# Performance work log

Hardware: AMD Instinct MI355X
Metric: run time of the kernel (lower is better)

## Reference

```python
import jax, jax.numpy as jnp
import numpy as np

B, T, F = 512, 1024, 8
H1, H2 = 70, 21   # '80k' config, bidirectional
D1, D2 = 30, 20


def _u(key, shape, fan):
    s = 1.0 / np.sqrt(fan)
    return jax.random.uniform(key, shape, jnp.float32, -s, s)


def setup_inputs() -> dict:
    key = jax.random.key(0)
    ks = iter(jax.random.split(key, 32))
    inp = {"x": jax.random.normal(next(ks), (B, T, F), jnp.float32)}
    # LSTM layer 1 (input F -> H1), forward and backward directions; torch gate order i,f,g,o
    for d in ("f", "b"):
        inp[f"w_ih1_{d}"] = _u(next(ks), (4 * H1, F), H1)
        inp[f"w_hh1_{d}"] = _u(next(ks), (4 * H1, H1), H1)
        inp[f"b_ih1_{d}"] = _u(next(ks), (4 * H1,), H1)
        inp[f"b_hh1_{d}"] = _u(next(ks), (4 * H1,), H1)
    # LSTM layer 2 (input 2*H1 -> H2)
    for d in ("f", "b"):
        inp[f"w_ih2_{d}"] = _u(next(ks), (4 * H2, 2 * H1), H2)
        inp[f"w_hh2_{d}"] = _u(next(ks), (4 * H2, H2), H2)
        inp[f"b_ih2_{d}"] = _u(next(ks), (4 * H2,), H2)
        inp[f"b_hh2_{d}"] = _u(next(ks), (4 * H2,), H2)
    # Dense head: 2*H2 -> D1 -> D2 -> 1
    inp["d1_w"] = _u(next(ks), (D1, 2 * H2), 2 * H2)
    inp["d1_b"] = _u(next(ks), (D1,), 2 * H2)
    inp["d2_w"] = _u(next(ks), (D2, D1), D1)
    inp["d2_b"] = _u(next(ks), (D2,), D1)
    inp["out_w"] = _u(next(ks), (1, D2), D2)
    inp["out_b"] = _u(next(ks), (1,), D2)
    return inp


def _lstm_dir(x, w_ih, w_hh, b_ih, b_hh, reverse):
    # x: [B, T, Fin]; torch LSTM gate order: i, f, g, o
    if reverse:
        x = x[:, ::-1]
    H = w_hh.shape[1]
    pre = jnp.einsum('btf,gf->btg', x, w_ih) + b_ih + b_hh  # [B, T, 4H]
    pre_t = jnp.moveaxis(pre, 1, 0)                          # [T, B, 4H]

    def step(carry, p):
        h, c = carry
        g = p + h @ w_hh.T
        i, f, gg, o = jnp.split(g, 4, axis=-1)
        c = jax.nn.sigmoid(f) * c + jax.nn.sigmoid(i) * jnp.tanh(gg)
        h = jax.nn.sigmoid(o) * jnp.tanh(c)
        return (h, c), h

    init = (jnp.zeros((x.shape[0], H), x.dtype), jnp.zeros((x.shape[0], H), x.dtype))
    _, hs = jax.lax.scan(step, init, pre_t)
    hs = jnp.moveaxis(hs, 0, 1)  # [B, T, H]
    if reverse:
        hs = hs[:, ::-1]
    return hs


def _bilstm(x, wf, uf, bif, bhf, wb, ub, bib, bhb):
    return jnp.concatenate([
        _lstm_dir(x, wf, uf, bif, bhf, reverse=False),
        _lstm_dir(x, wb, ub, bib, bhb, reverse=True),
    ], axis=-1)


def reference(x,
              w_ih1_f, w_hh1_f, b_ih1_f, b_hh1_f,
              w_ih1_b, w_hh1_b, b_ih1_b, b_hh1_b,
              w_ih2_f, w_hh2_f, b_ih2_f, b_hh2_f,
              w_ih2_b, w_hh2_b, b_ih2_b, b_hh2_b,
              d1_w, d1_b, d2_w, d2_b, out_w, out_b):
    h = _bilstm(x, w_ih1_f, w_hh1_f, b_ih1_f, b_hh1_f,
                w_ih1_b, w_hh1_b, b_ih1_b, b_hh1_b)   # [B, T, 2*H1]
    h = _bilstm(h, w_ih2_f, w_hh2_f, b_ih2_f, b_hh2_f,
                w_ih2_b, w_hh2_b, b_ih2_b, b_hh2_b)   # [B, T, 2*H2]
    h = jax.nn.relu(h @ d1_w.T + d1_b)
    h = jax.nn.relu(h @ d2_w.T + d2_b)
    return h @ out_w.T + out_b                          # [B, T, 1]
```

## Files before the change

### kernel.cpp

```cpp
#include <hip/hip_runtime.h>


typedef _Float16 v2f16 __attribute__((ext_vector_type(2)));
typedef _Float16 v4h   __attribute__((ext_vector_type(4)));
typedef _Float16 v8h   __attribute__((ext_vector_type(8)));
typedef float    f32x4 __attribute__((ext_vector_type(4)));

__device__ __forceinline__ float fdot2(v2f16 a, v2f16 b, float c) {
  return __builtin_amdgcn_fdot2(a, b, c, false);
}
#if __has_builtin(__builtin_amdgcn_rcpf)
__device__ __forceinline__ float rcpf(float x) { return __builtin_amdgcn_rcpf(x); }
#else
__device__ __forceinline__ float rcpf(float x) { return 1.f / x; }
#endif
__device__ __forceinline__ float ex2(float v) {
#if __has_builtin(__builtin_amdgcn_exp2f)
  return __builtin_amdgcn_exp2f(v);
#else
  return __expf(v * 0.6931471805599453f);
#endif
}
__device__ __forceinline__ float dpp_xor1(float v) {
  return __builtin_bit_cast(float,
      __builtin_amdgcn_update_dpp(0, __builtin_bit_cast(int, v),
                                  0xB1 , 0xF, 0xF, true));
}

__device__ __forceinline__ void lds_barrier() {
  asm volatile("s_waitcnt lgkmcnt(0)" ::: "memory");
  __builtin_amdgcn_s_barrier();
  __builtin_amdgcn_sched_barrier(0);
}

#define LOG2E  1.4426950408889634f
#define LOG2E2 2.8853900817779268f

#define O_W1M  0u
#define O_WP2  110592u
#define O_W2M  118656u
#define O_BIAS 177792u
#define O_DATA 178496u

__global__ void pack_kernel(const float* __restrict__ wihf, const float* __restrict__ whhf,
                            const float* __restrict__ wihb, const float* __restrict__ whhb,
                            const float* __restrict__ b1if, const float* __restrict__ b1hf,
                            const float* __restrict__ b1ib, const float* __restrict__ b1hb,
                            const float* __restrict__ wih2f, const float* __restrict__ wih2b,
                            const float* __restrict__ whh2f, const float* __restrict__ whh2b,
                            const float* __restrict__ bif, const float* __restrict__ bhf,
                            const float* __restrict__ bib, const float* __restrict__ bhb,
                            char* __restrict__ ws) {
  _Float16* w1m = (_Float16*)(ws + O_W1M);
  _Float16* wp2 = (_Float16*)(ws + O_WP2);
  _Float16* w2m = (_Float16*)(ws + O_W2M);
  float* biasc = (float*)(ws + O_BIAS);
  int idx = blockIdx.x * 256 + threadIdx.x;
  if (idx < 55296) {
    int d = idx / 27648, rem = idx % 27648, rp = rem / 96, k = rem % 96;
    int u = rp >> 2, g = rp & 3;
    const float* wih = d ? wihb : wihf;
    const float* whh = d ? whhb : whhf;
    const float* bi = d ? b1ib : b1if;
    const float* bh = d ? b1hb : b1hf;
    float v = 0.f;
    if (u < 70) {
      int src = g * 70 + u;
      float scale = (g == 2) ? LOG2E2 : LOG2E;
      if (k < 8) v = wih[src * 8 + k] * scale;
      else if (k < 78) v = whh[src * 70 + (k - 8)] * scale;
      else if (k == 78) v = (bi[src] + bh[src]) * scale;
    }
    w1m[idx] = (_Float16)v;
  } else if (idx < 59328) {
    int j = idx - 55296;
    int d = j / 2016, rem = j % 2016, r = rem / 24, k = rem % 24;
    const float* whh = d ? whh2b : whh2f;
    float scale = (r / 21 == 2) ? LOG2E2 : LOG2E;
    wp2[j] = (_Float16)((k < 21) ? whh[r * 21 + k] * scale : 0.f);
  } else if (idx < 88896) {
    int j = idx - 59328;
    int n = j / 168, k = j % 168;
    float v = 0.f;
    if (n < 168 && k < 140) {
      int d = n / 84, m = n % 84, u = m >> 2, g = m & 3;
      const float* wih = d ? wih2b : wih2f;
      float scale = (g == 2) ? LOG2E2 : LOG2E;
      v = wih[(g * 21 + u) * 140 + k] * scale;
    }
    w2m[j] = (_Float16)v;
  } else if (idx < 89072) {
    int n = idx - 88896;
    float v = 0.f;
    if (n < 168) {
      int d = n / 84, m = n % 84, u = m >> 2, g = m & 3;
      const float* bi = d ? bib : bif;
      const float* bh = d ? bhb : bhf;
      float scale = (g == 2) ? LOG2E2 : LOG2E;
      v = (bi[g * 21 + u] + bh[g * 21 + u]) * scale;
    }
    biasc[n] = v;
  }
}

__global__ __launch_bounds__(1024) void lstm1_kernel(
    const float* __restrict__ x,
    const _Float16* __restrict__ w1m,
    _Float16* __restrict__ h1, int b0, int nb) {
  __shared__ __align__(16) _Float16 km[2][16][104];
  const int tid = threadIdx.x;
  const int w = tid >> 6, lane = tid & 63;
  const int q = lane >> 4, bc = lane & 15;
  const int d = blockIdx.y;
  const int blg = blockIdx.x * 16;
  const int gb0 = b0 + blg;

  for (int i = tid; i < 2 * 16 * 104; i += 1024) ((_Float16*)km)[i] = (_Float16)0.f;

  const bool ldr = (w == 15);
  const bool two = (w < 2) || (w == 14);
  const int T0 = (w < 2) ? 2 * w : (w == 14 ? 16 : w + 2);

  v8h af[2][3];
  if (!ldr) {
#pragma unroll
    for (int kc = 0; kc < 3; ++kc)
      af[0][kc] = *(const v8h*)&w1m[(size_t)(d * 288 + T0 * 16 + bc) * 96 + kc * 32 + q * 8];
    if (two) {
#pragma unroll
      for (int kc = 0; kc < 3; ++kc)
        af[1][kc] = *(const v8h*)&w1m[(size_t)(d * 288 + (T0 + 1) * 16 + bc) * 96 + kc * 32 + q * 8];
    }
  }

  __syncthreads();

  if (tid < 16) {
    km[0][tid][78] = (_Float16)1.f;
    km[1][tid][78] = (_Float16)1.f;
  }
  const bool xlane = ldr && (lane < 32);
  const int xb = lane >> 1, xhalf = lane & 1;
  float4 xa, xb4, xc, xd;
  const float* xp = nullptr;
  const ptrdiff_t xstep = d ? -8 : 8;
  if (xlane) {
    const float* xrow = &x[((size_t)(gb0 + xb) * 1024) * 8 + xhalf * 4];
    int t0 = d ? 1023 : 0;
    float4 xv = *(const float4*)&xrow[(size_t)t0 * 8];
    v4h xh; xh[0] = (_Float16)xv.x; xh[1] = (_Float16)xv.y;
    xh[2] = (_Float16)xv.z; xh[3] = (_Float16)xv.w;
    *(v4h*)&km[0][xb][xhalf * 4] = xh;
    xa  = *(const float4*)&xrow[(size_t)(d ? 1022 : 1) * 8];
    xb4 = *(const float4*)&xrow[(size_t)(d ? 1021 : 2) * 8];
    xc  = *(const float4*)&xrow[(size_t)(d ? 1020 : 3) * 8];
    xd  = *(const float4*)&xrow[(size_t)(d ? 1019 : 4) * 8];
    xp  = &xrow[(size_t)(d ? 1018 : 5) * 8];
  }
  float c0 = 0.f, c1 = 0.f;
  int s = 0;
  __syncthreads();

#define GATE(Ai, ci, U)                                                      \
    {                                                                        \
      float ei = ex2(-Ai[0]);                                                \
      float ef = ex2(-Ai[1]);                                                \
      float eg = ex2(-Ai[2]);                                                \
      float eo = ex2(-Ai[3]);                                                \
      float sf = rcpf(1.f + ef);                                             \
      float ig = (1.f - eg) * rcpf((1.f + ei) * (1.f + eg));                 \
      ci = fmaf(sf, ci, ig);                                                 \
      float cl = fminf(fmaxf(ci, -14.f), 14.f);                              \
      float ec = ex2(cl * -LOG2E2);                                          \
      float hv = (1.f - ec) * rcpf((1.f + eo) * (1.f + ec));                 \
      if ((U) < 70) {                                                        \
        _Float16 hh = (_Float16)hv;                                          \
        km[nxt][bc][8 + (U)] = hh;                                           \
        h1[rowb + (U)] = hh;                                                 \
      }                                                                      \
    }

#define STEP1(XR)                                                            \
  {                                                                          \
    const int cur = s & 1, nxt = cur ^ 1;                                    \
    if (!ldr) {                                                              \
      v8h bf0 = *(const v8h*)&km[cur][bc][q * 8];                            \
      v8h bf1 = *(const v8h*)&km[cur][bc][32 + q * 8];                       \
      v8h bf2 = *(const v8h*)&km[cur][bc][64 + q * 8];                       \
      f32x4 z4 = (f32x4){0.f, 0.f, 0.f, 0.f};                                \
      f32x4 A0 = __builtin_amdgcn_mfma_f32_16x16x32_f16(af[0][0], bf0, z4, 0, 0, 0); \
      f32x4 A1 = z4;                                                         \
      if (two) A1 = __builtin_amdgcn_mfma_f32_16x16x32_f16(af[1][0], bf0, z4, 0, 0, 0); \
      A0 = __builtin_amdgcn_mfma_f32_16x16x32_f16(af[0][1], bf1, A0, 0, 0, 0); \
      if (two) A1 = __builtin_amdgcn_mfma_f32_16x16x32_f16(af[1][1], bf1, A1, 0, 0, 0); \
      A0 = __builtin_amdgcn_mfma_f32_16x16x32_f16(af[0][2], bf2, A0, 0, 0, 0); \
      if (two) A1 = __builtin_amdgcn_mfma_f32_16x16x32_f16(af[1][2], bf2, A1, 0, 0, 0); \
      const int te = d ? (1023 - s) : s;                                     \
      const size_t rowb = ((size_t)te * nb + blg + bc) * 176 + d * 70;       \
      GATE(A0, c0, T0 * 4 + q)                                               \
      if (two) GATE(A1, c1, (T0 + 1) * 4 + q)                                \
    } else if (xlane) {                                                      \
      if (s < 1023) {                                                        \
        v4h xh; xh[0] = (_Float16)XR.x; xh[1] = (_Float16)XR.y;              \
        xh[2] = (_Float16)XR.z; xh[3] = (_Float16)XR.w;                      \
        *(v4h*)&km[nxt][xb][xhalf * 4] = xh;                                 \
      }                                                                      \
      if (s <= 1018) XR = *(const float4*)xp;                                \
      xp += xstep;                                                           \
    }                                                                        \
    ++s;                                                                     \
    lds_barrier();                                                           \
  }

#pragma unroll 1
  for (int it = 0; it < 256; ++it) {
    STEP1(xa)
    STEP1(xb4)
    STEP1(xc)
    STEP1(xd)
  }
#undef STEP1
#undef GATE
}

__global__ __launch_bounds__(256) void pre2_kernel(
    _Float16* __restrict__ h1, const char* __restrict__ ws) {
  const _Float16* w2m = (const _Float16*)(ws + O_W2M);
  const float* biasc = (const float*)(ws + O_BIAS);
  __shared__ _Float16 Al[64][184];
  __shared__ float Bl[176];
  const int tid = threadIdx.x;
  const int r0 = blockIdx.x * 64;
#pragma unroll
  for (int i = 0; i < 6; ++i) {
    int cid = i * 256 + tid;
    if (cid < 1408) {
      int row = cid / 22, ch = cid % 22;
      *(v8h*)&Al[row][ch * 8] = *(const v8h*)&h1[(size_t)(r0 + row) * 176 + ch * 8];
    }
  }
  if (tid < 176) Bl[tid] = biasc[tid];
  __syncthreads();

  const int wv = tid >> 6, lane = tid & 63;
  const int ml = lane & 15, kq = lane >> 4;
  v8h af[5];
#pragma unroll
  for (int k = 0; k < 4; ++k)
    af[k] = *(const v8h*)&Al[wv * 16 + ml][k * 32 + kq * 8];
  {
    v8h a4 = *(const v8h*)&Al[wv * 16 + ml][128 + kq * 8];
    if (kq >= 2) {
#pragma unroll
      for (int j = 0; j < 8; ++j) a4[j] = (_Float16)0.f;
    } else if (kq == 1) {
#pragma unroll
      for (int j = 4; j < 8; ++j) a4[j] = (_Float16)0.f;
    }
    af[4] = a4;
  }

  const v8h* wg = (const v8h*)w2m;
  f32x4 acc[11];
#pragma unroll
  for (int ct = 0; ct < 11; ++ct) acc[ct] = (f32x4){0.f, 0.f, 0.f, 0.f};

  v8h bc[5], bn[5];
#pragma unroll
  for (int k = 0; k < 5; ++k) bn[k] = wg[(size_t)ml * 21 + k * 4 + kq];
#pragma unroll
  for (int ct = 0; ct < 11; ++ct) {
#pragma unroll
    for (int k = 0; k < 5; ++k) bc[k] = bn[k];
    if (ct < 10) {
#pragma unroll
      for (int k = 0; k < 5; ++k) bn[k] = wg[(size_t)((ct + 1) * 16 + ml) * 21 + k * 4 + kq];
    }
#pragma unroll
    for (int k = 0; k < 5; ++k)
      acc[ct] = __builtin_amdgcn_mfma_f32_16x16x32_f16(af[k], bc[k], acc[ct], 0, 0, 0);
  }
  __syncthreads();
#pragma unroll
  for (int ct = 0; ct < 11; ++ct) {
#pragma unroll
    for (int r = 0; r < 4; ++r) {
      int row = wv * 16 + kq * 4 + r, col = ct * 16 + ml;
      Al[row][col] = (_Float16)(acc[ct][r] + Bl[col]);
    }
  }
  __syncthreads();
#pragma unroll
  for (int i = 0; i < 6; ++i) {
    int cid = i * 256 + tid;
    if (cid < 1408) {
      int row = cid / 22, ch = cid % 22;
      *(v8h*)&h1[(size_t)(r0 + row) * 176 + ch * 8] = *(const v8h*)&Al[row][ch * 8];
    }
  }
}

__global__ __launch_bounds__(64) void lstm2_kernel(
    const _Float16* __restrict__ pre2, const _Float16* __restrict__ wp2,
    _Float16* __restrict__ h2, int nb) {
  __shared__ __align__(16) _Float16 kv[2][32];
  const int lane = threadIdx.x;
  const int bl = blockIdx.x;
  const int d = blockIdx.y;
  const int u = lane >> 1, p = lane & 1;
  const bool active = lane < 42;

  ((_Float16*)kv)[lane] = (_Float16)0.f;

  v2f16 w0[12], w1[12];
  if (active) {
    const v8h* wr0 = (const v8h*)&wp2[(d * 84 + (2 * p) * 21 + u) * 24];
    const v8h* wr1 = (const v8h*)&wp2[(d * 84 + (2 * p + 1) * 21 + u) * 24];
#pragma unroll
    for (int ch = 0; ch < 3; ++ch) {
      v8h a = wr0[ch], b = wr1[ch];
#pragma unroll
      for (int q = 0; q < 4; ++q) {
        v2f16 t0; t0[0] = a[2 * q]; t0[1] = a[2 * q + 1]; w0[ch * 4 + q] = t0;
        v2f16 t1; t1[0] = b[2 * q]; t1[1] = b[2 * q + 1]; w1[ch * 4 + q] = t1;
      }
    }
  }
  const int cp = d * 84 + u * 4 + 2 * p;
  const ptrdiff_t dlt = (ptrdiff_t)(d ? -nb : nb) * 176;
  const _Float16* pp = pre2 + ((size_t)(d ? 1023 : 0) * (size_t)nb + bl) * 176;

  v2f16 pa = *(const v2f16*)(pp + cp);
  v2f16 pb = *(const v2f16*)(pp + dlt + cp);
  v2f16 pc = *(const v2f16*)(pp + 2 * dlt + cp);
  v2f16 pd = *(const v2f16*)(pp + 3 * dlt + cp);
  v2f16 pe = *(const v2f16*)(pp + 4 * dlt + cp);
  v2f16 pg = *(const v2f16*)(pp + 5 * dlt + cp);
  v2f16 ph = *(const v2f16*)(pp + 6 * dlt + cp);
  v2f16 pi = *(const v2f16*)(pp + 7 * dlt + cp);
  const _Float16* pf = pp + 8 * dlt;

  float cc = 0.f;
  int s = 0;

#define L2STEP(P)                                                           \
  {                                                                         \
    const int cur = s & 1, nxt = cur ^ 1;                                   \
    float A0v = (float)P[0], A1v = (float)P[1];                             \
    const float4* kp = (const float4*)&kv[cur][0];                          \
    float4 q0 = kp[0], q1 = kp[1], q2 = kp[2];                              \
    float x0 = A0v, x1 = 0.f, x2 = 0.f, x3 = 0.f;                           \
    float z0 = A1v, z1 = 0.f, z2 = 0.f, z3 = 0.f;                           \
    x0 = fdot2(__builtin_bit_cast(v2f16, q0.x), w0[0], x0);                 \
    x1 = fdot2(__builtin_bit_cast(v2f16, q0.y), w0[1], x1);                 \
    x2 = fdot2(__builtin_bit_cast(v2f16, q0.z), w0[2], x2);                 \
    x3 = fdot2(__builtin_bit_cast(v2f16, q0.w), w0[3], x3);                 \
    x0 = fdot2(__builtin_bit_cast(v2f16, q1.x), w0[4], x0);                 \
    x1 = fdot2(__builtin_bit_cast(v2f16, q1.y), w0[5], x1);                 \
    x2 = fdot2(__builtin_bit_cast(v2f16, q1.z), w0[6], x2);                 \
    x3 = fdot2(__builtin_bit_cast(v2f16, q1.w), w0[7], x3);                 \
    x0 = fdot2(__builtin_bit_cast(v2f16, q2.x), w0[8], x0);                 \
    x1 = fdot2(__builtin_bit_cast(v2f16, q2.y), w0[9], x1);                 \
    x2 = fdot2(__builtin_bit_cast(v2f16, q2.z), w0[10], x2);                \
    x3 = fdot2(__builtin_bit_cast(v2f16, q2.w), w0[11], x3);                \
    z0 = fdot2(__builtin_bit_cast(v2f16, q0.x), w1[0], z0);                 \
    z1 = fdot2(__builtin_bit_cast(v2f16, q0.y), w1[1], z1);                 \
    z2 = fdot2(__builtin_bit_cast(v2f16, q0.z), w1[2], z2);                 \
    z3 = fdot2(__builtin_bit_cast(v2f16, q0.w), w1[3], z3);                 \
    z0 = fdot2(__builtin_bit_cast(v2f16, q1.x), w1[4], z0);                 \
    z1 = fdot2(__builtin_bit_cast(v2f16, q1.y), w1[5], z1);                 \
    z2 = fdot2(__builtin_bit_cast(v2f16, q1.z), w1[6], z2);                 \
    z3 = fdot2(__builtin_bit_cast(v2f16, q1.w), w1[7], z3);                 \
    z0 = fdot2(__builtin_bit_cast(v2f16, q2.x), w1[8], z0);                 \
    z1 = fdot2(__builtin_bit_cast(v2f16, q2.y), w1[9], z1);                 \
    z2 = fdot2(__builtin_bit_cast(v2f16, q2.z), w1[10], z2);                \
    z3 = fdot2(__builtin_bit_cast(v2f16, q2.w), w1[11], z3);                \
    float A = (x0 + x1) + (x2 + x3), Bv = (z0 + z1) + (z2 + z3);            \
            \
    float r0v = rcpf(1.f + ex2(-A));                                        \
    float Y0 = p ? fmaf(2.f, r0v, -1.f) : r0v;                              \
    float Y1 = rcpf(1.f + ex2(-Bv));                                        \
    float Zs = dpp_xor1(Y0);                                                \
    float Ws = dpp_xor1(Y1);                                                \
    float ai = p ? Zs : Y0;                                                 \
    float af = p ? Ws : Y1;                                                 \
    float ag = p ? Y0 : Zs;                                                 \
    float ao = p ? Y1 : Ws;                                                 \
    cc = fmaf(af, cc, ai * ag);                                             \
    float tc = fmaf(2.f, rcpf(1.f + ex2(cc * -LOG2E2)), -1.f);              \
    float hv = ao * tc;                                                     \
    if (active && p == 0) {                                                 \
      _Float16 hh = (_Float16)hv;                                           \
      int te = d ? (1023 - s) : s;                                          \
      kv[nxt][u] = hh;                                                      \
      h2[((size_t)te * nb + bl) * 48 + d * 21 + u] = hh;                    \
    }                                                                       \
    if (s < 1016) P = *(const v2f16*)(pf + cp);                             \
    pf += dlt;                                                              \
    ++s;                                                                    \
  }

#pragma unroll 1
  for (int it = 0; it < 128; ++it) {
    L2STEP(pa)
    L2STEP(pb)
    L2STEP(pc)
    L2STEP(pd)
    L2STEP(pe)
    L2STEP(pg)
    L2STEP(ph)
    L2STEP(pi)
  }
#undef L2STEP
}

__global__ __launch_bounds__(256) void head_kernel(
    const _Float16* __restrict__ h2,
    const float* __restrict__ d1w, const float* __restrict__ d1b,
    const float* __restrict__ d2w, const float* __restrict__ d2b,
    const float* __restrict__ ow, const float* __restrict__ ob,
    float* __restrict__ out, int b0, int lognb) {
  int n = blockIdx.x * 256 + threadIdx.x;
  int t = n >> lognb, bl = n & ((1 << lognb) - 1);
  const v8h* hp = (const v8h*)&h2[(size_t)n * 48];
  float in[48];
#pragma unroll
  for (int i = 0; i < 6; ++i) {
    v8h hc = hp[i];
#pragma unroll
    for (int j = 0; j < 8; ++j) in[i * 8 + j] = (float)hc[j];
  }
  float a1[30];
#pragma unroll
  for (int cc = 0; cc < 30; ++cc) {
    float a = d1b[cc];
#pragma unroll
    for (int k = 0; k < 42; ++k) a += in[k] * d1w[cc * 42 + k];
    a1[cc] = fmaxf(a, 0.f);
  }
  float a2[20];
#pragma unroll
  for (int cc = 0; cc < 20; ++cc) {
    float a = d2b[cc];
#pragma unroll
    for (int k = 0; k < 30; ++k) a += a1[k] * d2w[cc * 30 + k];
    a2[cc] = fmaxf(a, 0.f);
  }
  float o = ob[0];
#pragma unroll
  for (int k = 0; k < 20; ++k) o += a2[k] * ow[k];
  out[(size_t)(b0 + bl) * 1024 + t] = o;
}

extern "C" void kernel_launch(void* const* d_in, const int* in_sizes, int n_in,
                              void* d_out, int out_size, void* d_ws, size_t ws_size,
                              hipStream_t stream) {
  const float* x = (const float*)d_in[0];
  const float* wih1f = (const float*)d_in[1];
  const float* whh1f = (const float*)d_in[2];
  const float* bih1f = (const float*)d_in[3];
  const float* bhh1f = (const float*)d_in[4];
  const float* wih1b = (const float*)d_in[5];
  const float* whh1b = (const float*)d_in[6];
  const float* bih1b = (const float*)d_in[7];
  const float* bhh1b = (const float*)d_in[8];
  const float* wih2f = (const float*)d_in[9];
  const float* whh2f = (const float*)d_in[10];
  const float* bih2f = (const float*)d_in[11];
  const float* bhh2f = (const float*)d_in[12];
  const float* wih2b = (const float*)d_in[13];
  const float* whh2b = (const float*)d_in[14];
  const float* bih2b = (const float*)d_in[15];
  const float* bhh2b = (const float*)d_in[16];
  const float* d1w = (const float*)d_in[17];
  const float* d1b = (const float*)d_in[18];
  const float* d2w = (const float*)d_in[19];
  const float* d2b = (const float*)d_in[20];
  const float* ow = (const float*)d_in[21];
  const float* ob = (const float*)d_in[22];
  float* out = (float*)d_out;
  char* wsb = (char*)d_ws;

  const int cands[6] = {1, 2, 4, 8, 16, 32};
  int nslice = 32;
  for (int i = 0; i < 6; ++i) {
    size_t rows = (size_t)(512 / cands[i]) * 1024;
    if (O_DATA + rows * 448 <= ws_size) { nslice = cands[i]; break; }
  }
  const int nb = 512 / nslice;
  int lognb = 0; while ((1 << lognb) < nb) ++lognb;
  const size_t rows = (size_t)nb * 1024;

  _Float16* w1m = (_Float16*)(wsb + O_W1M);
  _Float16* wp2 = (_Float16*)(wsb + O_WP2);
  _Float16* h1  = (_Float16*)(wsb + O_DATA);
  _Float16* h2  = (_Float16*)(wsb + O_DATA + rows * 352);

  pack_kernel<<<348, 256, 0, stream>>>(wih1f, whh1f, wih1b, whh1b,
                                       bih1f, bhh1f, bih1b, bhh1b,
                                       wih2f, wih2b, whh2f, whh2b,
                                       bih2f, bhh2f, bih2b, bhh2b, wsb);

  for (int s = 0; s < nslice; ++s) {
    const int b0 = s * nb;
    lstm1_kernel<<<dim3(nb / 16, 2), 1024, 0, stream>>>(x, w1m, h1, b0, nb);
    pre2_kernel<<<nb * 16, 256, 0, stream>>>(h1, wsb);
    lstm2_kernel<<<dim3(nb, 2), 64, 0, stream>>>(h1, wp2, h2, nb);
    head_kernel<<<nb * 4, 256, 0, stream>>>(h2, d1w, d1b, d2w, d2b, ow, ob,
                                            out, b0, lognb);
  }
}
```

Baseline: 1.212 ms.

## Fuse forward and backward LSTM2 directions into one wavefront per batch row

The layer-2 LSTM kernel now runs both directions inside one 64-lane block instead of one block per direction. Each step interleaves two independent recurrences, so the dot products and activations of one direction can hide the latency of the other. This halves the block count and doubles the register weights per lane. That lowers parallelism across CUs and may raise register pressure.

New measurement: 1.288 ms. 6.3% more time.

```diff
diff --git a/kernel.cpp b/kernel.cpp
--- a/kernel.cpp
+++ b/kernel.cpp
@@ -303,115 +303,147 @@
 __global__ __launch_bounds__(64) void lstm2_kernel(
     const _Float16* __restrict__ pre2, const _Float16* __restrict__ wp2,
     _Float16* __restrict__ h2, int nb) {
-  __shared__ __align__(16) _Float16 kv[2][32];
+  __shared__ __align__(16) _Float16 kv[2][2][32];
   const int lane = threadIdx.x;
   const int bl = blockIdx.x;
-  const int d = blockIdx.y;
   const int u = lane >> 1, p = lane & 1;
   const bool active = lane < 42;
 
   ((_Float16*)kv)[lane] = (_Float16)0.f;
-
-  v2f16 w0[12], w1[12];
+  ((_Float16*)kv)[64 + lane] = (_Float16)0.f;
+
+  v2f16 wA0[12], wA1[12], wB0[12], wB1[12];
   if (active) {
-    const v8h* wr0 = (const v8h*)&wp2[(d * 84 + (2 * p) * 21 + u) * 24];
-    const v8h* wr1 = (const v8h*)&wp2[(d * 84 + (2 * p + 1) * 21 + u) * 24];
-#pragma unroll
-    for (int ch = 0; ch < 3; ++ch) {
-      v8h a = wr0[ch], b = wr1[ch];
-#pragma unroll
-      for (int q = 0; q < 4; ++q) {
-        v2f16 t0; t0[0] = a[2 * q]; t0[1] = a[2 * q + 1]; w0[ch * 4 + q] = t0;
-        v2f16 t1; t1[0] = b[2 * q]; t1[1] = b[2 * q + 1]; w1[ch * 4 + q] = t1;
+#pragma unroll
+    for (int dd = 0; dd < 2; ++dd) {
+      const v8h* wr0 = (const v8h*)&wp2[(dd * 84 + (2 * p) * 21 + u) * 24];
+      const v8h* wr1 = (const v8h*)&wp2[(dd * 84 + (2 * p + 1) * 21 + u) * 24];
+#pragma unroll
+      for (int ch = 0; ch < 3; ++ch) {
+        v8h a = wr0[ch], b = wr1[ch];
+#pragma unroll
+        for (int q = 0; q < 4; ++q) {
+          v2f16 t0; t0[0] = a[2 * q]; t0[1] = a[2 * q + 1];
+          v2f16 t1; t1[0] = b[2 * q]; t1[1] = b[2 * q + 1];
+          if (dd == 0) { wA0[ch * 4 + q] = t0; wA1[ch * 4 + q] = t1; }
+          else         { wB0[ch * 4 + q] = t0; wB1[ch * 4 + q] = t1; }
+        }
       }
     }
   }
-  const int cp = d * 84 + u * 4 + 2 * p;
-  const ptrdiff_t dlt = (ptrdiff_t)(d ? -nb : nb) * 176;
-  const _Float16* pp = pre2 + ((size_t)(d ? 1023 : 0) * (size_t)nb + bl) * 176;
-
-  v2f16 pa = *(const v2f16*)(pp + cp);
-  v2f16 pb = *(const v2f16*)(pp + dlt + cp);
-  v2f16 pc = *(const v2f16*)(pp + 2 * dlt + cp);
-  v2f16 pd = *(const v2f16*)(pp + 3 * dlt + cp);
-  v2f16 pe = *(const v2f16*)(pp + 4 * dlt + cp);
-  v2f16 pg = *(const v2f16*)(pp + 5 * dlt + cp);
-  v2f16 ph = *(const v2f16*)(pp + 6 * dlt + cp);
-  v2f16 pi = *(const v2f16*)(pp + 7 * dlt + cp);
-  const _Float16* pf = pp + 8 * dlt;
-
-  float cc = 0.f;
+  const int cp = u * 4 + 2 * p;
+  const ptrdiff_t dP = (ptrdiff_t)nb * 176;
+  const _Float16* pf0 = pre2 + (size_t)bl * 176 + cp;
+  const _Float16* pf1 = pre2 + ((size_t)1023 * nb + bl) * 176 + 84 + cp;
+
+  v2f16 a0 = *(const v2f16*)(pf0);
+  v2f16 b0 = *(const v2f16*)(pf0 + dP);
+  v2f16 c0 = *(const v2f16*)(pf0 + 2 * dP);
+  v2f16 d0 = *(const v2f16*)(pf0 + 3 * dP);
+  v2f16 e0 = *(const v2f16*)(pf0 + 4 * dP);
+  v2f16 f0 = *(const v2f16*)(pf0 + 5 * dP);
+  v2f16 g0 = *(const v2f16*)(pf0 + 6 * dP);
+  v2f16 h0 = *(const v2f16*)(pf0 + 7 * dP);
+  v2f16 a1 = *(const v2f16*)(pf1);
+  v2f16 b1 = *(const v2f16*)(pf1 - dP);
+  v2f16 c1 = *(const v2f16*)(pf1 - 2 * dP);
+  v2f16 d1 = *(const v2f16*)(pf1 - 3 * dP);
+  v2f16 e1 = *(const v2f16*)(pf1 - 4 * dP);
+  v2f16 f1 = *(const v2f16*)(pf1 - 5 * dP);
+  v2f16 g1 = *(const v2f16*)(pf1 - 6 * dP);
+  v2f16 h1v = *(const v2f16*)(pf1 - 7 * dP);
+  pf0 += 8 * dP;
+  pf1 -= 8 * dP;
+
+  float cc0 = 0.f, cc1 = 0.f;
   int s = 0;
 
-#define L2STEP(P)                                                           \
+#define DOT12(acc0, acc1, acc2, acc3, qq0, qq1, qq2, W)                     \
+    acc0 = fdot2(__builtin_bit_cast(v2f16, qq0.x), W[0], acc0);             \
+    acc1 = fdot2(__builtin_bit_cast(v2f16, qq0.y), W[1], acc1);             \
+    acc2 = fdot2(__builtin_bit_cast(v2f16, qq0.z), W[2], acc2);             \
+    acc3 = fdot2(__builtin_bit_cast(v2f16, qq0.w), W[3], acc3);             \
+    acc0 = fdot2(__builtin_bit_cast(v2f16, qq1.x), W[4], acc0);             \
+    acc1 = fdot2(__builtin_bit_cast(v2f16, qq1.y), W[5], acc1);             \
+    acc2 = fdot2(__builtin_bit_cast(v2f16, qq1.z), W[6], acc2);             \
+    acc3 = fdot2(__builtin_bit_cast(v2f16, qq1.w), W[7], acc3);             \
+    acc0 = fdot2(__builtin_bit_cast(v2f16, qq2.x), W[8], acc0);             \
+    acc1 = fdot2(__builtin_bit_cast(v2f16, qq2.y), W[9], acc1);             \
+    acc2 = fdot2(__builtin_bit_cast(v2f16, qq2.z), W[10], acc2);            \
+    acc3 = fdot2(__builtin_bit_cast(v2f16, qq2.w), W[11], acc3);
+
+#define L2D(P0, P1)                                                         \
   {                                                                         \
     const int cur = s & 1, nxt = cur ^ 1;                                   \
-    float A0v = (float)P[0], A1v = (float)P[1];                             \
-    const float4* kp = (const float4*)&kv[cur][0];                          \
-    float4 q0 = kp[0], q1 = kp[1], q2 = kp[2];                              \
-    float x0 = A0v, x1 = 0.f, x2 = 0.f, x3 = 0.f;                           \
-    float z0 = A1v, z1 = 0.f, z2 = 0.f, z3 = 0.f;                           \
-    x0 = fdot2(__builtin_bit_cast(v2f16, q0.x), w0[0], x0);                 \
-    x1 = fdot2(__builtin_bit_cast(v2f16, q0.y), w0[1], x1);                 \
-    x2 = fdot2(__builtin_bit_cast(v2f16, q0.z), w0[2], x2);                 \
-    x3 = fdot2(__builtin_bit_cast(v2f16, q0.w), w0[3], x3);                 \
-    x0 = fdot2(__builtin_bit_cast(v2f16, q1.x), w0[4], x0);                 \
-    x1 = fdot2(__builtin_bit_cast(v2f16, q1.y), w0[5], x1);                 \
-    x2 = fdot2(__builtin_bit_cast(v2f16, q1.z), w0[6], x2);                 \
-    x3 = fdot2(__builtin_bit_cast(v2f16, q1.w), w0[7], x3);                 \
-    x0 = fdot2(__builtin_bit_cast(v2f16, q2.x), w0[8], x0);                 \
-    x1 = fdot2(__builtin_bit_cast(v2f16, q2.y), w0[9], x1);                 \
-    x2 = fdot2(__builtin_bit_cast(v2f16, q2.z), w0[10], x2);                \
-    x3 = fdot2(__builtin_bit_cast(v2f16, q2.w), w0[11], x3);                \
-    z0 = fdot2(__builtin_bit_cast(v2f16, q0.x), w1[0], z0);                 \
-    z1 = fdot2(__builtin_bit_cast(v2f16, q0.y), w1[1], z1);                 \
-    z2 = fdot2(__builtin_bit_cast(v2f16, q0.z), w1[2], z2);                 \
-    z3 = fdot2(__builtin_bit_cast(v2f16, q0.w), w1[3], z3);                 \
-    z0 = fdot2(__builtin_bit_cast(v2f16, q1.x), w1[4], z0);                 \
-    z1 = fdot2(__builtin_bit_cast(v2f16, q1.y), w1[5], z1);                 \
-    z2 = fdot2(__builtin_bit_cast(v2f16, q1.z), w1[6], z2);                 \
-    z3 = fdot2(__builtin_bit_cast(v2f16, q1.w), w1[7], z3);                 \
-    z0 = fdot2(__builtin_bit_cast(v2f16, q2.x), w1[8], z0);                 \
-    z1 = fdot2(__builtin_bit_cast(v2f16, q2.y), w1[9], z1);                 \
-    z2 = fdot2(__builtin_bit_cast(v2f16, q2.z), w1[10], z2);                \
-    z3 = fdot2(__builtin_bit_cast(v2f16, q2.w), w1[11], z3);                \
-    float A = (x0 + x1) + (x2 + x3), Bv = (z0 + z1) + (z2 + z3);            \
-            \
-    float r0v = rcpf(1.f + ex2(-A));                                        \
-    float Y0 = p ? fmaf(2.f, r0v, -1.f) : r0v;                              \
-    float Y1 = rcpf(1.f + ex2(-Bv));                                        \
-    float Zs = dpp_xor1(Y0);                                                \
-    float Ws = dpp_xor1(Y1);                                                \
-    float ai = p ? Zs : Y0;                                                 \
-    float af = p ? Ws : Y1;                                                 \
-    float ag = p ? Y0 : Zs;                                                 \
-    float ao = p ? Y1 : Ws;                                                 \
-    cc = fmaf(af, cc, ai * ag);                                             \
-    float tc = fmaf(2.f, rcpf(1.f + ex2(cc * -LOG2E2)), -1.f);              \
-    float hv = ao * tc;                                                     \
+    const float4* k0 = (const float4*)&kv[0][cur][0];                       \
+    const float4* k1 = (const float4*)&kv[1][cur][0];                       \
+    float4 q00 = k0[0], q01 = k0[1], q02 = k0[2];                           \
+    float4 q10 = k1[0], q11 = k1[1], q12 = k1[2];                           \
+    float x0 = (float)P0[0], x1 = 0.f, x2 = 0.f, x3 = 0.f;                  \
+    float z0 = (float)P0[1], z1 = 0.f, z2 = 0.f, z3 = 0.f;                  \
+    float y0 = (float)P1[0], y1 = 0.f, y2 = 0.f, y3 = 0.f;                  \
+    float t0 = (float)P1[1], t1 = 0.f, t2 = 0.f, t3 = 0.f;                  \
+    DOT12(x0, x1, x2, x3, q00, q01, q02, wA0)                               \
+    DOT12(y0, y1, y2, y3, q10, q11, q12, wB0)                               \
+    DOT12(z0, z1, z2, z3, q00, q01, q02, wA1)                               \
+    DOT12(t0, t1, t2, t3, q10, q11, q12, wB1)                               \
+    float Af = (x0 + x1) + (x2 + x3), Bf = (z0 + z1) + (z2 + z3);           \
+    float Ab = (y0 + y1) + (y2 + y3), Bb = (t0 + t1) + (t2 + t3);           \
+                                                                  \
+    float r0f = rcpf(1.f + ex2(-Af));                                       \
+    float Y0f = p ? fmaf(2.f, r0f, -1.f) : r0f;                             \
+    float Y1f = rcpf(1.f + ex2(-Bf));                                       \
+    float Zsf = dpp_xor1(Y0f);                                              \
+    float Wsf = dpp_xor1(Y1f);                                              \
+    float aif = p ? Zsf : Y0f;                                              \
+    float aff = p ? Wsf : Y1f;                                              \
+    float agf = p ? Y0f : Zsf;                                              \
+    float aof = p ? Y1f : Wsf;                                              \
+    cc0 = fmaf(aff, cc0, aif * agf);                                        \
+    float tcf = fmaf(2.f, rcpf(1.f + ex2(cc0 * -LOG2E2)), -1.f);            \
+    float hvf = aof * tcf;                                                  \
+                                                                  \
+    float r0b = rcpf(1.f + ex2(-Ab));                                       \
+    float Y0b = p ? fmaf(2.f, r0b, -1.f) : r0b;                             \
+    float Y1b = rcpf(1.f + ex2(-Bb));                                       \
+    float Zsb = dpp_xor1(Y0b);                                              \
+    float Wsb = dpp_xor1(Y1b);                                              \
+    float aib = p ? Zsb : Y0b;                                              \
+    float afb = p ? Wsb : Y1b;                                              \
+    float agb = p ? Y0b : Zsb;                                              \
+    float aob = p ? Y1b : Wsb;                                              \
+    cc1 = fmaf(afb, cc1, aib * agb);                                        \
+    float tcb = fmaf(2.f, rcpf(1.f + ex2(cc1 * -LOG2E2)), -1.f);            \
+    float hvb = aob * tcb;                                                  \
     if (active && p == 0) {                                                 \
-      _Float16 hh = (_Float16)hv;                                           \
-      int te = d ? (1023 - s) : s;                                          \
-      kv[nxt][u] = hh;                                                      \
-      h2[((size_t)te * nb + bl) * 48 + d * 21 + u] = hh;                    \
+      _Float16 hf = (_Float16)hvf, hb = (_Float16)hvb;                      \
+      kv[0][nxt][u] = hf;                                                   \
+      kv[1][nxt][u] = hb;                                                   \
+      h2[((size_t)s * nb + bl) * 48 + u] = hf;                              \
+      h2[((size_t)(1023 - s) * nb + bl) * 48 + 21 + u] = hb;                \
     }                                                                       \
-    if (s < 1016) P = *(const v2f16*)(pf + cp);                             \
-    pf += dlt;                                                              \
+    if (s < 1016) {                                                         \
+      P0 = *(const v2f16*)pf0;                                              \
+      P1 = *(const v2f16*)pf1;                                              \
+    }                                                                       \
+    pf0 += dP;                                                              \
+    pf1 -= dP;                                                              \
     ++s;                                                                    \
   }
 
 #pragma unroll 1
   for (int it = 0; it < 128; ++it) {
-    L2STEP(pa)
-    L2STEP(pb)
-    L2STEP(pc)
-    L2STEP(pd)
-    L2STEP(pe)
-    L2STEP(pg)
-    L2STEP(ph)
-    L2STEP(pi)
-  }
-#undef L2STEP
+    L2D(a0, a1)
+    L2D(b0, b1)
+    L2D(c0, c1)
+    L2D(d0, d1)
+    L2D(e0, e1)
+    L2D(f0, f1)
+    L2D(g0, g1)
+    L2D(h0, h1v)
+  }
+#undef L2D
+#undef DOT12
 }
 
 __global__ __launch_bounds__(256) void head_kernel(
@@ -505,7 +537,7 @@
     const int b0 = s * nb;
     lstm1_kernel<<<dim3(nb / 16, 2), 1024, 0, stream>>>(x, w1m, h1, b0, nb);
     pre2_kernel<<<nb * 16, 256, 0, stream>>>(h1, wsb);
-    lstm2_kernel<<<dim3(nb, 2), 64, 0, stream>>>(h1, wp2, h2, nb);
+    lstm2_kernel<<<nb, 64, 0, stream>>>(h1, wp2, h2, nb);
     head_kernel<<<nb * 4, 256, 0, stream>>>(h2, d1w, d1b, d2w, d2b, ow, ob,
                                             out, b0, lognb);
   }
```
